# Kernel tuning notes

Measured on AMD Instinct MI355X. Metric: run time of the kernel, lower is better.

Reference implementation:

```python
import jax, jax.numpy as jnp
import numpy as np
from jax import lax

COST_CLASS, COST_BBOX, COST_GIOU = 1.0, 5.0, 2.0


def box_cxcywh_to_xyxy(b):
    cx, cy, w, h = b[..., 0], b[..., 1], b[..., 2], b[..., 3]
    return jnp.stack([cx - 0.5 * w, cy - 0.5 * h, cx + 0.5 * w, cy + 0.5 * h], axis=-1)


def generalized_box_iou(boxes1, boxes2):
    # boxes1: [Q,4] xyxy, boxes2: [T,4] xyxy -> [Q,T]
    area1 = (boxes1[:, 2] - boxes1[:, 0]) * (boxes1[:, 3] - boxes1[:, 1])
    area2 = (boxes2[:, 2] - boxes2[:, 0]) * (boxes2[:, 3] - boxes2[:, 1])
    lt = jnp.maximum(boxes1[:, None, :2], boxes2[None, :, :2])  # [Q,T,2]
    rb = jnp.minimum(boxes1[:, None, 2:], boxes2[None, :, 2:])
    wh = jnp.clip(rb - lt, 0.0)
    inter = wh[..., 0] * wh[..., 1]
    union = area1[:, None] + area2[None, :] - inter
    iou = inter / union
    # smallest enclosing box
    lt_c = jnp.minimum(boxes1[:, None, :2], boxes2[None, :, :2])
    rb_c = jnp.maximum(boxes1[:, None, 2:], boxes2[None, :, 2:])
    wh_c = jnp.clip(rb_c - lt_c, 0.0)
    area_c = wh_c[..., 0] * wh_c[..., 1]
    return iou - (area_c - union) / area_c


def cost_matrix(logits, pboxes, labels, tboxes):
    # logits [Q,C], pboxes [Q,4], labels [T], tboxes [T,4] -> C [Q,T]
    prob = jax.nn.softmax(logits, axis=-1)
    cost_class = -prob[:, labels]                                  # [Q,T]
    cost_bbox = jnp.sum(jnp.abs(pboxes[:, None] - tboxes[None]), axis=-1)  # L1 cdist
    giou = generalized_box_iou(box_cxcywh_to_xyxy(pboxes), box_cxcywh_to_xyxy(tboxes))
    return COST_CLASS * cost_class + COST_BBOX * cost_bbox - COST_GIOU * giou


def greedy_match(C):
    # sequential greedy global-argmin matching, T steps (T <= Q)
    Q, T = C.shape

    def step(Cc, _):
        flat = jnp.argmin(Cc)
        i, j = flat // T, flat % T
        Cc = Cc.at[i, :].set(jnp.inf).at[:, j].set(jnp.inf)
        return Cc, (i.astype(jnp.int32), j.astype(jnp.int32))

    _, (src, tgt) = lax.scan(step, C, None, length=T)
    return src, tgt


def setup_inputs() -> dict:
    key = jax.random.key(0)
    k1, k2, k3, k4 = jax.random.split(key, 4)
    B, Q, C, T = 64, 900, 91, 128
    return {
        "pred_logits": jax.random.normal(k1, (B, Q, C), dtype=jnp.float32),
        "pred_boxes": jax.random.uniform(k2, (B, Q, 4), dtype=jnp.float32),
        "tgt_labels": jax.random.randint(k3, (B, T), 0, C, dtype=jnp.int32),
        "tgt_boxes": jax.random.uniform(k4, (B, T, 4), dtype=jnp.float32),
    }


def reference(pred_logits, pred_boxes, tgt_labels, tgt_boxes):
    C = jax.vmap(cost_matrix)(pred_logits, pred_boxes, tgt_labels, tgt_boxes)  # [B,Q,T]
    src_idx, tgt_idx = jax.vmap(greedy_match)(C)  # [B,T] each
    return src_idx, tgt_idx, C
```

## Files before the change

### kernel.cpp

```cpp
#include <hip/hip_runtime.h>
#include <cstdint>
#include <math.h>

#define NQ 900
#define NT 128
#define NC 91
#define KROWS 15
#define NCH 10

typedef unsigned long long u64;
typedef unsigned int u32;

__device__ __forceinline__ u32 fmono(float f){
  u32 u = __float_as_uint(f);
  return (u & 0x80000000u) ? ~u : (u | 0x80000000u);
}

__global__ void softmax_stats_kernel(const float* __restrict__ logits,
                                     float* __restrict__ stats, int nrows){
  int gw   = (int)((blockIdx.x * blockDim.x + threadIdx.x) >> 6);
  int lane = threadIdx.x & 63;
  if (gw >= nrows) return;
  const float* row = logits + (size_t)gw * NC;
  float v0 = (lane      < NC) ? row[lane]      : -INFINITY;
  float v1 = (lane + 64 < NC) ? row[lane + 64] : -INFINITY;
  float m = fmaxf(v0, v1);
  #pragma unroll
  for (int off = 32; off; off >>= 1) m = fmaxf(m, __shfl_xor(m, off));
  float s = ((lane < NC) ? expf(v0 - m) : 0.0f)
          + ((lane + 64 < NC) ? expf(v1 - m) : 0.0f);
  #pragma unroll
  for (int off = 32; off; off >>= 1) s += __shfl_xor(s, off);
  if (lane == 0){ stats[2*gw] = m; stats[2*gw+1] = s; }
}

__global__ void cost_kernel(const float* __restrict__ logits,
                            const float* __restrict__ pboxes,
                            const int*   __restrict__ labels,
                            const float* __restrict__ tboxes,
                            const float* __restrict__ stats,
                            float* __restrict__ Cout, int total){
#pragma clang fp contract(off)
  int idx = blockIdx.x * blockDim.x + threadIdx.x;
  if (idx >= total) return;
  int t  = idx & (NT - 1);
  int bq = idx >> 7;
  int b  = bq / NQ;

  int   lab = labels[b*NT + t];
  float l   = logits[(size_t)bq*NC + lab];
  float m   = stats[2*bq], s = stats[2*bq+1];
  float cclass = -(expf(l - m) / s);

  const float* pb = pboxes + (size_t)bq*4;
  const float* tb = tboxes + ((size_t)b*NT + t)*4;
  float pcx = pb[0], pcy = pb[1], pw = pb[2], ph = pb[3];
  float tcx = tb[0], tcy = tb[1], tw = tb[2], th = tb[3];

  float cbbox = ((fabsf(pcx-tcx) + fabsf(pcy-tcy)) + fabsf(pw-tw)) + fabsf(ph-th);

  float px0 = pcx - 0.5f*pw, py0 = pcy - 0.5f*ph;
  float px1 = pcx + 0.5f*pw, py1 = pcy + 0.5f*ph;
  float tx0 = tcx - 0.5f*tw, ty0 = tcy - 0.5f*th;
  float tx1 = tcx + 0.5f*tw, ty1 = tcy + 0.5f*th;

  float area1 = (px1 - px0) * (py1 - py0);
  float area2 = (tx1 - tx0) * (ty1 - ty0);
  float ltx = fmaxf(px0, tx0), lty = fmaxf(py0, ty0);
  float rbx = fminf(px1, tx1), rby = fminf(py1, ty1);
  float wx = fmaxf(rbx - ltx, 0.0f), wy = fmaxf(rby - lty, 0.0f);
  float inter = wx * wy;
  float uni   = (area1 + area2) - inter;
  float iou   = inter / uni;
  float cx0 = fminf(px0, tx0), cy0 = fminf(py0, ty0);
  float cx1 = fmaxf(px1, tx1), cy1 = fmaxf(py1, ty1);
  float cwx = fmaxf(cx1 - cx0, 0.0f), cwy = fmaxf(cy1 - cy0, 0.0f);
  float areac = cwx * cwy;
  float giou  = iou - (areac - uni) / areac;

  float cost = (cclass + 5.0f*cbbox) - 2.0f*giou;
  Cout[idx] = cost;
}

__global__ __launch_bounds__(128) void colmin_kernel(const float* __restrict__ Cmat,
                                                     u64* __restrict__ colmin){
  int b  = blockIdx.x / NCH;
  int ch = blockIdx.x - b * NCH;
  int t  = threadIdx.x;
  const float* Cb = Cmat + (size_t)b * NQ * NT + t;
  int r0 = ch * (NQ / NCH);
  u64 best = ~0ull;
  #pragma unroll 6
  for (int r = r0; r < r0 + NQ/NCH; ++r){
    float v = Cb[(size_t)r * NT];
    u64 k = ((u64)fmono(v) << 32) | (u32)r;
    best = k < best ? k : best;
  }
  atomicMin(&colmin[b * NT + t], best);
}

__global__ __launch_bounds__(64) void greedy_kernel(const float* __restrict__ Cmat,
                                                    const u64* __restrict__ colmin,
                                                    float* __restrict__ outsrc,
                                                    float* __restrict__ outtgt){
  const int b    = blockIdx.x;
  const int lane = threadIdx.x;
  const float* Cb = Cmat + (size_t)b * NQ * NT;
  const u32 colA = 2*lane, colB = 2*lane + 1;

  ulonglong2 kk = ((const ulonglong2*)(colmin + (size_t)b * NT))[lane];
  u64 keyA, keyB;
  {
    u32 mono = (u32)(kk.x >> 32), row = (u32)kk.x & 0x3FFu;
    keyA = ((u64)mono << 20) | (row << 7) | colA;
    mono = (u32)(kk.y >> 32); row = (u32)kk.y & 0x3FFu;
    keyB = ((u64)mono << 20) | (row << 7) | colB;
  }

  u64 rd[KROWS];
  #pragma unroll
  for (int k = 0; k < KROWS; ++k) rd[k] = 0;

  for (int step = 0; step < NT; ++step){
    u64 g;
    while (true){
      u64 cand = keyA < keyB ? keyA : keyB;
      #pragma unroll
      for (int off = 1; off < 64; off <<= 1){
        u64 o = __shfl_xor(cand, off);
        cand = o < cand ? o : cand;
      }
      if (!((cand >> 17) & 1ull)){ g = cand; break; }

      int jj = (int)(cand & 0x7Fu);
      u64 best = ~0ull;
      #pragma unroll
      for (int k = 0; k < KROWS; ++k){
        int r = lane + 64*k;
        u64 c2 = ~0ull;
        if (r < NQ){
          float v = Cb[(size_t)r * NT + jj];
          bool dead = ((rd[k] >> lane) & 1ull) != 0ull;
          c2 = dead ? ~0ull : (((u64)fmono(v) << 32) | (u32)r);
        }
        best = c2 < best ? c2 : best;
      }
      #pragma unroll
      for (int off = 1; off < 64; off <<= 1){
        u64 o = __shfl_xor(best, off);
        best = o < best ? o : best;
      }
      if (lane == (jj >> 1)){
        u32 mono = (u32)(best >> 32), row = (u32)best & 0x3FFu;
        u64 nk = ((u64)mono << 20) | (row << 7) | (u32)jj;
        if (jj & 1) keyB = nk; else keyA = nk;
      }
    }

    int i = (int)((g >> 7) & 0x3FFu);
    int j = (int)(g & 0x7Fu);
    if (lane == 0){
      outsrc[b*NT + step] = (float)i;
      outtgt[b*NT + step] = (float)j;
    }

    #pragma unroll
    for (int k = 0; k < KROWS; ++k)
      if ((i >> 6) == k) rd[k] |= (1ull << (i & 63));

    if (lane == (j >> 1)){
      if (j & 1) keyB = ~0ull; else keyA = ~0ull;
    }
    if (((keyA >> 7) & 0x3FFu) == (u32)i) keyA |= (1ull << 17);
    if (((keyB >> 7) & 0x3FFu) == (u32)i) keyB |= (1ull << 17);
  }
}

extern "C" void kernel_launch(void* const* d_in, const int* in_sizes, int n_in,
                              void* d_out, int out_size, void* d_ws, size_t ws_size,
                              hipStream_t stream){
  const float* logits = (const float*)d_in[0];
  const float* pboxes = (const float*)d_in[1];
  const int*   labels = (const int*)  d_in[2];
  const float* tboxes = (const float*)d_in[3];
  int B = in_sizes[0] / (NQ * NC);

  float* out    = (float*)d_out;
  float* outsrc = out;
  float* outtgt = out + (size_t)B * NT;
  float* Cmat   = out + (size_t)2 * B * NT;

  float* stats  = (float*)d_ws;
  u64*   colmin = (u64*)d_ws;

  int nrows = B * NQ;
  int blocks0 = (nrows + 3) / 4;
  softmax_stats_kernel<<<blocks0, 256, 0, stream>>>(logits, stats, nrows);

  int total = B * NQ * NT;
  cost_kernel<<<(total + 255) / 256, 256, 0, stream>>>(logits, pboxes, labels,
                                                       tboxes, stats, Cmat, total);

  hipMemsetAsync(colmin, 0xFF, (size_t)B * NT * sizeof(u64), stream);
  colmin_kernel<<<B * NCH, 128, 0, stream>>>(Cmat, colmin);

  greedy_kernel<<<B, 64, 0, stream>>>(Cmat, colmin, outsrc, outtgt);
}
```

Before: 275.0 us.

## Fuse softmax stats into cost kernel, drop atomics, use DPP float argmin in greedy

Softmax row statistics are now computed inside the cost kernel, two waves per block, and shared through LDS, which removes a separate kernel launch and the stats round trip. The column-min pass writes per-chunk partials instead of doing atomicMin after a memset, and the greedy kernel reduces those partials itself. The greedy loop replaces 64-bit shuffle reductions with a float DPP min plus a ballot and readlane for the index, falling back to a second DPP pass only when values tie. In exchange there is a block-wide sync in the cost kernel, and tie-breaking and the stale-flag encoding are now more intricate.

After: 246.0 us. -10.6%, faster.

```diff
diff --git a/kernel.cpp b/kernel.cpp
--- a/kernel.cpp
+++ b/kernel.cpp
@@ -15,41 +15,65 @@
   u32 u = __float_as_uint(f);
   return (u & 0x80000000u) ? ~u : (u | 0x80000000u);
 }
-
-__global__ void softmax_stats_kernel(const float* __restrict__ logits,
-                                     float* __restrict__ stats, int nrows){
-  int gw   = (int)((blockIdx.x * blockDim.x + threadIdx.x) >> 6);
-  int lane = threadIdx.x & 63;
-  if (gw >= nrows) return;
-  const float* row = logits + (size_t)gw * NC;
-  float v0 = (lane      < NC) ? row[lane]      : -INFINITY;
-  float v1 = (lane + 64 < NC) ? row[lane + 64] : -INFINITY;
-  float m = fmaxf(v0, v1);
-  #pragma unroll
-  for (int off = 32; off; off >>= 1) m = fmaxf(m, __shfl_xor(m, off));
-  float s = ((lane < NC) ? expf(v0 - m) : 0.0f)
-          + ((lane + 64 < NC) ? expf(v1 - m) : 0.0f);
-  #pragma unroll
-  for (int off = 32; off; off >>= 1) s += __shfl_xor(s, off);
-  if (lane == 0){ stats[2*gw] = m; stats[2*gw+1] = s; }
-}
-
-__global__ void cost_kernel(const float* __restrict__ logits,
-                            const float* __restrict__ pboxes,
-                            const int*   __restrict__ labels,
-                            const float* __restrict__ tboxes,
-                            const float* __restrict__ stats,
-                            float* __restrict__ Cout, int total){
+__device__ __forceinline__ float fmono_inv(u32 m){
+  u32 u = (m & 0x80000000u) ? (m & 0x7FFFFFFFu) : ~m;
+  return __uint_as_float(u);
+}
+
+__device__ __forceinline__ u32 wave_argmin(float lv, u32 lm, float* gout){
+  float x = lv;
+  #define FSTG(C,RM) { int t_ = __builtin_amdgcn_update_dpp(__float_as_int(x), __float_as_int(x), C, RM, 0xf, false); x = fminf(x, __int_as_float(t_)); }
+  FSTG(0x111,0xf) FSTG(0x112,0xf) FSTG(0x114,0xf) FSTG(0x118,0xf)
+  FSTG(0x142,0xa) FSTG(0x143,0xc)
+  #undef FSTG
+  float gv = __int_as_float(__builtin_amdgcn_readlane(__float_as_int(x), 63));
+  *gout = gv;
+  u64 tie = __ballot(lv == gv);
+  if (__popcll(tie) == 1){
+    int w = (int)__ffsll((long long)tie) - 1;
+    return (u32)__builtin_amdgcn_readlane((int)lm, w);
+  }
+  u32 m = (lv == gv) ? lm : 0xFFFFFFFFu;
+  #define USTG(C,RM) { u32 t_ = (u32)__builtin_amdgcn_update_dpp((int)m, (int)m, C, RM, 0xf, false); m = t_ < m ? t_ : m; }
+  USTG(0x111,0xf) USTG(0x112,0xf) USTG(0x114,0xf) USTG(0x118,0xf)
+  USTG(0x142,0xa) USTG(0x143,0xc)
+  #undef USTG
+  return (u32)__builtin_amdgcn_readlane((int)m, 63);
+}
+
+__global__ __launch_bounds__(256) void cost_kernel(const float* __restrict__ logits,
+                                                   const float* __restrict__ pboxes,
+                                                   const int*   __restrict__ labels,
+                                                   const float* __restrict__ tboxes,
+                                                   float* __restrict__ Cout){
 #pragma clang fp contract(off)
-  int idx = blockIdx.x * blockDim.x + threadIdx.x;
-  if (idx >= total) return;
-  int t  = idx & (NT - 1);
-  int bq = idx >> 7;
-  int b  = bq / NQ;
+  int blk = blockIdx.x, tid = threadIdx.x;
+  int idx = blk * 256 + tid;
+  int t   = idx & (NT - 1);
+  int bq  = idx >> 7;
+  int b   = bq / NQ;
+  int wid = tid >> 6, lane = tid & 63;
+
+  __shared__ float sm_m[2], sm_s[2];
+  if ((wid & 1) == 0){
+    int r = blk * 2 + (wid >> 1);
+    const float* row = logits + (size_t)r * NC;
+    float v0 = (lane      < NC) ? row[lane]      : -INFINITY;
+    float v1 = (lane + 64 < NC) ? row[lane + 64] : -INFINITY;
+    float m = fmaxf(v0, v1);
+    #pragma unroll
+    for (int off = 32; off; off >>= 1) m = fmaxf(m, __shfl_xor(m, off));
+    float s = ((lane < NC) ? expf(v0 - m) : 0.0f)
+            + ((lane + 64 < NC) ? expf(v1 - m) : 0.0f);
+    #pragma unroll
+    for (int off = 32; off; off >>= 1) s += __shfl_xor(s, off);
+    if (lane == 0){ sm_m[wid >> 1] = m; sm_s[wid >> 1] = s; }
+  }
+  __syncthreads();
+  float m = sm_m[tid >> 7], s = sm_s[tid >> 7];
 
   int   lab = labels[b*NT + t];
   float l   = logits[(size_t)bq*NC + lab];
-  float m   = stats[2*bq], s = stats[2*bq+1];
   float cclass = -(expf(l - m) / s);
 
   const float* pb = pboxes + (size_t)bq*4;
@@ -83,7 +107,7 @@
 }
 
 __global__ __launch_bounds__(128) void colmin_kernel(const float* __restrict__ Cmat,
-                                                     u64* __restrict__ colmin){
+                                                     u64* __restrict__ part){
   int b  = blockIdx.x / NCH;
   int ch = blockIdx.x - b * NCH;
   int t  = threadIdx.x;
@@ -96,11 +120,11 @@
     u64 k = ((u64)fmono(v) << 32) | (u32)r;
     best = k < best ? k : best;
   }
-  atomicMin(&colmin[b * NT + t], best);
+  part[((size_t)b * NCH + ch) * NT + t] = best;
 }
 
 __global__ __launch_bounds__(64) void greedy_kernel(const float* __restrict__ Cmat,
-                                                    const u64* __restrict__ colmin,
+                                                    const u64* __restrict__ part,
                                                     float* __restrict__ outsrc,
                                                     float* __restrict__ outtgt){
   const int b    = blockIdx.x;
@@ -108,57 +132,54 @@
   const float* Cb = Cmat + (size_t)b * NQ * NT;
   const u32 colA = 2*lane, colB = 2*lane + 1;
 
-  ulonglong2 kk = ((const ulonglong2*)(colmin + (size_t)b * NT))[lane];
-  u64 keyA, keyB;
-  {
-    u32 mono = (u32)(kk.x >> 32), row = (u32)kk.x & 0x3FFu;
-    keyA = ((u64)mono << 20) | (row << 7) | colA;
-    mono = (u32)(kk.y >> 32); row = (u32)kk.y & 0x3FFu;
-    keyB = ((u64)mono << 20) | (row << 7) | colB;
-  }
+  u64 kA = ~0ull, kB = ~0ull;
+  #pragma unroll
+  for (int ch = 0; ch < NCH; ++ch){
+    ulonglong2 p = ((const ulonglong2*)(part + ((size_t)b * NCH + ch) * NT))[lane];
+    kA = p.x < kA ? p.x : kA;
+    kB = p.y < kB ? p.y : kB;
+  }
+  float vA = fmono_inv((u32)(kA >> 32));
+  float vB = fmono_inv((u32)(kB >> 32));
+  u32 mA = ((((u32)kA) & 0x3FFu) << 7) | colA;
+  u32 mB = ((((u32)kB) & 0x3FFu) << 7) | colB;
 
   u64 rd[KROWS];
   #pragma unroll
   for (int k = 0; k < KROWS; ++k) rd[k] = 0;
 
   for (int step = 0; step < NT; ++step){
-    u64 g;
+    u32 gm;
     while (true){
-      u64 cand = keyA < keyB ? keyA : keyB;
-      #pragma unroll
-      for (int off = 1; off < 64; off <<= 1){
-        u64 o = __shfl_xor(cand, off);
-        cand = o < cand ? o : cand;
-      }
-      if (!((cand >> 17) & 1ull)){ g = cand; break; }
-
-      int jj = (int)(cand & 0x7Fu);
-      u64 best = ~0ull;
+      bool bsel = (vB < vA) || ((vB == vA) && (mB < mA));
+      float lv = bsel ? vB : vA;
+      u32   lm = bsel ? mB : mA;
+      float gv;
+      u32 g = wave_argmin(lv, lm, &gv);
+      if (!(g >> 24)){ gm = g; break; }
+
+      int jj = (int)(g & 0x7Fu);
+      float w1 = INFINITY; u32 s1 = 0;
       #pragma unroll
       for (int k = 0; k < KROWS; ++k){
         int r = lane + 64*k;
-        u64 c2 = ~0ull;
         if (r < NQ){
           float v = Cb[(size_t)r * NT + jj];
           bool dead = ((rd[k] >> lane) & 1ull) != 0ull;
-          c2 = dead ? ~0ull : (((u64)fmono(v) << 32) | (u32)r);
+          v = dead ? INFINITY : v;
+          if (v < w1){ w1 = v; s1 = (u32)r; }
         }
-        best = c2 < best ? c2 : best;
       }
-      #pragma unroll
-      for (int off = 1; off < 64; off <<= 1){
-        u64 o = __shfl_xor(best, off);
-        best = o < best ? o : best;
-      }
+      float rgv;
+      u32 rrow = wave_argmin(w1, s1, &rgv);
       if (lane == (jj >> 1)){
-        u32 mono = (u32)(best >> 32), row = (u32)best & 0x3FFu;
-        u64 nk = ((u64)mono << 20) | (row << 7) | (u32)jj;
-        if (jj & 1) keyB = nk; else keyA = nk;
+        if (jj & 1){ vB = rgv; mB = (rrow << 7) | (u32)jj; }
+        else       { vA = rgv; mA = (rrow << 7) | (u32)jj; }
       }
     }
 
-    int i = (int)((g >> 7) & 0x3FFu);
-    int j = (int)(g & 0x7Fu);
+    int i = (int)((gm >> 7) & 0x3FFu);
+    int j = (int)(gm & 0x7Fu);
     if (lane == 0){
       outsrc[b*NT + step] = (float)i;
       outtgt[b*NT + step] = (float)j;
@@ -169,10 +190,11 @@
       if ((i >> 6) == k) rd[k] |= (1ull << (i & 63));
 
     if (lane == (j >> 1)){
-      if (j & 1) keyB = ~0ull; else keyA = ~0ull;
+      if (j & 1){ vB = INFINITY; mB = 0x00FFFFFFu & ~(1u<<24); mB = 0x00FFFFFFu; }
+      else      { vA = INFINITY; mA = 0x00FFFFFFu; }
     }
-    if (((keyA >> 7) & 0x3FFu) == (u32)i) keyA |= (1ull << 17);
-    if (((keyB >> 7) & 0x3FFu) == (u32)i) keyB |= (1ull << 17);
+    if (((mA >> 7) & 0x3FFu) == (u32)i) mA |= (1u << 24);
+    if (((mB >> 7) & 0x3FFu) == (u32)i) mB |= (1u << 24);
   }
 }
 
@@ -190,19 +212,12 @@
   float* outtgt = out + (size_t)B * NT;
   float* Cmat   = out + (size_t)2 * B * NT;
 
-  float* stats  = (float*)d_ws;
-  u64*   colmin = (u64*)d_ws;
-
-  int nrows = B * NQ;
-  int blocks0 = (nrows + 3) / 4;
-  softmax_stats_kernel<<<blocks0, 256, 0, stream>>>(logits, stats, nrows);
-
-  int total = B * NQ * NT;
-  cost_kernel<<<(total + 255) / 256, 256, 0, stream>>>(logits, pboxes, labels,
-                                                       tboxes, stats, Cmat, total);
-
-  hipMemsetAsync(colmin, 0xFF, (size_t)B * NT * sizeof(u64), stream);
-  colmin_kernel<<<B * NCH, 128, 0, stream>>>(Cmat, colmin);
-
-  greedy_kernel<<<B, 64, 0, stream>>>(Cmat, colmin, outsrc, outtgt);
-}
+  u64* part = (u64*)d_ws;
+
+  int nblk = (B * NQ) / 2;
+  cost_kernel<<<nblk, 256, 0, stream>>>(logits, pboxes, labels, tboxes, Cmat);
+
+  colmin_kernel<<<B * NCH, 128, 0, stream>>>(Cmat, part);
+
+  greedy_kernel<<<B, 64, 0, stream>>>(Cmat, part, outsrc, outtgt);
+}
```
